# Optimization experiments

Hardware: AMD Instinct MI355X
Metric: run time of the kernel (lower is better)

The kernel has to match this reference:

```python
import jax, jax.numpy as jnp
import numpy as np

B, CIN, H, W = 32, 1, 512, 512
PATCH = 16
PW, PH = H // PATCH, W // PATCH  # 32, 32
S = PW * PH                      # 1024 tokens
C = 256
L = 8
POOL = 4
OUT_IDX = (2, 4, 6)
EPS = 1e-5


def setup_inputs() -> dict:
    key = jax.random.key(0)
    ks = jax.random.split(key, 10)
    sc = 1.0 / np.sqrt(C).astype(np.float32)
    return {
        "image": jax.random.normal(ks[0], (B, CIN, H, W), jnp.float32),
        "conv_w": jax.random.normal(ks[1], (C, CIN), jnp.float32),
        "conv_b": jnp.zeros((C,), jnp.float32),
        "feat_w": jax.random.normal(ks[2], (C, C), jnp.float32) * sc,
        "feat_b": jnp.zeros((C,), jnp.float32),
        "ln_s": jnp.ones((L, C), jnp.float32),
        "ln_b": jnp.zeros((L, C), jnp.float32),
        "wq": jax.random.normal(ks[3], (L, C, C), jnp.float32) * sc,
        "bq": jnp.zeros((L, C), jnp.float32),
        "wk": jax.random.normal(ks[4], (L, C, C), jnp.float32) * sc,
        "bk": jnp.zeros((L, C), jnp.float32),
        "wv": jax.random.normal(ks[5], (L, C, C), jnp.float32) * sc,
        "bv": jnp.zeros((L, C), jnp.float32),
        "wf": jax.random.normal(ks[6], (L, C, C), jnp.float32) * sc,
        "bf": jnp.zeros((L, C), jnp.float32),
        "wa": jax.random.normal(ks[7], (L, C, 2 * C), jnp.float32) * sc,
        "ba": jnp.zeros((L, 2 * C), jnp.float32),
    }


def _to_spatial(t):  # [B,S,C] -> [B,C,PW,PH]
    return t.transpose(0, 2, 1).reshape(t.shape[0], C, PW, PH)


def _to_seq(t):  # [B,C,PW,PH] -> [B,S,C]
    return t.reshape(t.shape[0], C, S).transpose(0, 2, 1)


def _layernorm(x, s, b):
    mu = x.mean(-1, keepdims=True)
    var = x.var(-1, keepdims=True)
    return (x - mu) * jax.lax.rsqrt(var + EPS) * s + b


def _attention(x, Wq, bq, Wk, bk, Wv, bv):
    d = np.float32(1.0 / np.sqrt(C))
    Q = _to_spatial(jax.nn.sigmoid(x @ Wq + bq))
    K = _to_spatial(jax.nn.sigmoid(x @ Wk + bk))
    V = _to_spatial(jax.nn.sigmoid(x @ Wv + bv))
    # avg_pool2d with kernel (POOL, 1): pool rows of the patch grid
    qp = Q.reshape(B, C, PW // POOL, POOL, PH).mean(3)
    kp = K.reshape(B, C, PW // POOL, POOL, PH).mean(3)
    # dual softmax low-rank factorization, per channel
    Qk = jax.nn.softmax(d * jnp.einsum('ncik,ncjk->ncij', Q, kp), axis=-1)   # [B,C,PW,PW/POOL]
    Kq = jax.nn.softmax(d * jnp.einsum('ncik,ncjk->ncij', qp, K), axis=-1)   # [B,C,PW/POOL,PW]
    Kqv = jnp.einsum('ncik,nckj->ncij', Kq, V)                               # [B,C,PW/POOL,PH]
    return _to_seq(jnp.einsum('ncik,nckj->ncij', Qk, Kqv))                   # [B,S,C]


def _forward(image, conv_w, conv_b, feat_w, feat_b, ln_s, ln_b,
             wq, bq, wk, bk, wv, bv, wf, bf, wa, ba):
    # Conv2d(kernel=1, stride=patch) == strided subsample + 1x1 projection
    xs = image[:, :, ::PATCH, ::PATCH]                                       # [B,1,PW,PH]
    emb = jnp.einsum('bihw,oi->bohw', xs, conv_w) + conv_b[None, :, None, None]
    x = jnp.tanh(_to_seq(emb) @ feat_w + feat_b)                             # [B,S,C]
    hid, att = [], []
    for l in range(L):
        tn = _layernorm(x, ln_s[l], ln_b[l])
        a = _attention(tn, wq[l], bq[l], wk[l], bk[l], wv[l], bv[l])
        ta = x + a
        # FiLM adaptive norm: sigmoid linear -> interleaved (scale, shift) pairs
        sh = jax.nn.sigmoid(ta @ wa[l] + ba[l]).reshape(B, S, C, 2)
        tn2 = sh[..., 0] * ta + sh[..., 1]
        x = jax.nn.relu(tn2 @ wf[l] + bf[l]) + ta
        if l in OUT_IDX:
            hid.append(x)
            att.append(ta)
    # pack: [last; 3 intermediate hiddens; 3 attention residuals] -> [7,B,S,C]
    return jnp.concatenate([x[None], jnp.stack(hid), jnp.stack(att)], axis=0)


def reference(image, conv_w, conv_b, feat_w, feat_b, ln_s, ln_b,
              wq, bq, wk, bk, wv, bv, wf, bf, wa, ba):
    return _forward(image, conv_w, conv_b, feat_w, feat_b, ln_s, ln_b,
                    wq, bq, wk, bk, wv, bv, wf, bf, wa, ba)
```

## Files before the change

### kernel.cpp

```cpp
#include <hip/hip_runtime.h>
#include <hip/hip_bf16.h>
#include <cstdint>
#include <cstddef>

#define B_ 32
#define C_ 256
#define S_ 1024
#define L_ 8

typedef unsigned short bf16_t;
typedef __attribute__((ext_vector_type(8))) short s8v;
typedef __attribute__((ext_vector_type(4))) short s4v;
typedef __attribute__((ext_vector_type(4))) float f4v;

static __device__ __forceinline__ float b2f(bf16_t v) {
    unsigned int u = ((unsigned int)v) << 16;
    float f;
    __builtin_memcpy(&f, &u, 4);
    return f;
}
static __device__ __forceinline__ bf16_t f2b(float f) {
    unsigned int u;
    __builtin_memcpy(&u, &f, 4);
    u += 0x7fffu + ((u >> 16) & 1u);
    return (bf16_t)(u >> 16);
}
static __device__ __forceinline__ float sigmoidf_(float x) {
    return 1.0f / (1.0f + __expf(-x));
}
static __device__ __forceinline__ void gload_lds16(const void* g, void* l) {
    __builtin_amdgcn_global_load_lds((const __attribute__((address_space(1))) void*)g,
                                     (__attribute__((address_space(3))) void*)l, 16, 0, 0);
}


__global__ void make_xs_k(const float* __restrict__ img, float* __restrict__ xs) {
    int t = blockIdx.x * 256 + threadIdx.x;
    if (t >= B_ * S_) return;
    int b = t >> 10, s = t & 1023, i = s >> 5, k = s & 31;
    xs[t] = img[(size_t)b * 512 * 512 + (size_t)(i * 16) * 512 + k * 16];
}

__global__ void fuse_wb_k(const float* __restrict__ cw, const float* __restrict__ cb,
                          const float* __restrict__ fwm, const float* __restrict__ fbv,
                          float* __restrict__ fw, float* __restrict__ fb) {
    int c = threadIdx.x;
    float a = 0.f, bs = 0.f;
    for (int o = 0; o < C_; o++) {
        float f = fwm[o * C_ + c];
        a += cw[o] * f;
        bs += cb[o] * f;
    }
    fw[c] = a;
    fb[c] = bs + fbv[c];
}

__global__ __launch_bounds__(256) void wtrans_k(const float* __restrict__ wq, const float* __restrict__ wk,
                                                const float* __restrict__ wv, const float* __restrict__ wf,
                                                const float* __restrict__ wa, const float* __restrict__ ln_s,
                                                bf16_t* __restrict__ WT) {
    __shared__ float t[32][33];
    int z = blockIdx.z, l = z / 6, tp = z - l * 6;
    const float* src;
    int ld, cmul, coff;
    if (tp < 4) {
        const float* bases[4] = {wq, wk, wv, wf};
        src = bases[tp] + (size_t)l * 65536;
        ld = 256; cmul = 1; coff = 0;
    } else {
        src = wa + (size_t)l * 131072;
        ld = 512; cmul = 2; coff = tp - 4;
    }
    const float* g = ln_s + l * 256;
    bf16_t* dst = WT + ((size_t)l * 6 + tp) * 65536;
    int k0 = blockIdx.y * 32, m0 = blockIdx.x * 32;
    int tx = threadIdx.x & 31, ty = threadIdx.x >> 5;
#pragma unroll
    for (int r = 0; r < 4; ++r) {
        int k = k0 + ty + 8 * r;
        float v = src[(size_t)k * ld + (m0 + tx) * cmul + coff];
        if (tp < 3) v *= g[k];
        t[ty + 8 * r][tx] = v;
    }
    __syncthreads();
#pragma unroll
    for (int r = 0; r < 4; ++r)
        dst[(size_t)(m0 + ty + 8 * r) * 256 + k0 + tx] = f2b(t[tx][ty + 8 * r]);
}

__global__ __launch_bounds__(256) void colsum_k(const bf16_t* __restrict__ WT,
                                                const float* __restrict__ wq, const float* __restrict__ wk,
                                                const float* __restrict__ wv,
                                                const float* __restrict__ bq, const float* __restrict__ bk,
                                                const float* __restrict__ bv,
                                                const float* __restrict__ ln_b,
                                                float* __restrict__ csum, float* __restrict__ bias2) {
    int m = threadIdx.x, mat = blockIdx.x, l = blockIdx.y;
    const bf16_t* wt = WT + ((size_t)l * 6 + mat) * 65536 + (size_t)m * 256;
    float cs = 0.f;
    for (int k = 0; k < 256; k += 8) {
        s8v u = *(const s8v*)(wt + k);
#pragma unroll
        for (int j = 0; j < 8; ++j) cs += b2f((bf16_t)u[j]);
    }
    const float* worig = (mat == 0 ? wq : mat == 1 ? wk : wv) + (size_t)l * 65536;
    const float* borig = (mat == 0 ? bq : mat == 1 ? bk : bv) + l * 256;
    const float* lb = ln_b + l * 256;
    float bb = 0.f;
    for (int k = 0; k < 256; ++k) bb += lb[k] * worig[(size_t)k * 256 + m];
    int o = (l * 3 + mat) * 256 + m;
    csum[o] = cs;
    bias2[o] = bb + borig[m];
}

__global__ __launch_bounds__(256) void embed_k(const float* __restrict__ xs, const float* __restrict__ fw,
                                               const float* __restrict__ fb, bf16_t* __restrict__ X,
                                               float* __restrict__ rs, float* __restrict__ rsmu) {
    int wid = threadIdx.x >> 6, lane = threadIdx.x & 63;
    int row = blockIdx.x * 4 + wid;
    float xv = xs[row];
    f4v fwv = *(const f4v*)(fw + lane * 4);
    f4v fbv = *(const f4v*)(fb + lane * 4);
    s4v o;
    float sum = 0.f, sq = 0.f;
#pragma unroll
    for (int j = 0; j < 4; ++j) {
        float v = tanhf(xv * fwv[j] + fbv[j]);
        float vb = b2f(f2b(v));
        o[j] = (short)f2b(v);
        sum += vb;
        sq += vb * vb;
    }
    *(s4v*)(X + (size_t)row * 256 + lane * 4) = o;
#pragma unroll
    for (int off = 32; off > 0; off >>= 1) {
        sum += __shfl_xor(sum, off);
        sq += __shfl_xor(sq, off);
    }
    if (lane == 0) {
        float mu = sum * (1.f / 256.f);
        float var = sq * (1.f / 256.f) - mu * mu;
        float r = rsqrtf(var + 1e-5f);
        rs[row] = r;
        rsmu[row] = r * mu;
    }
}

__global__ __launch_bounds__(256) void stats_k(const bf16_t* __restrict__ X,
                                               float* __restrict__ rs, float* __restrict__ rsmu) {
    int wid = threadIdx.x >> 6, lane = threadIdx.x & 63;
    int row2 = blockIdx.x * 8 + wid * 2;
    s8v v = *(const s8v*)(X + (size_t)row2 * 256 + lane * 8);
    float sum = 0.f, sq = 0.f;
#pragma unroll
    for (int j = 0; j < 8; ++j) {
        float f = b2f((bf16_t)v[j]);
        sum += f;
        sq += f * f;
    }
#pragma unroll
    for (int off = 16; off > 0; off >>= 1) {
        sum += __shfl_xor(sum, off);
        sq += __shfl_xor(sq, off);
    }
    if ((lane & 31) == 0) {
        int row = row2 + (lane >> 5);
        float mu = sum * (1.f / 256.f);
        float var = sq * (1.f / 256.f) - mu * mu;
        float r = rsqrtf(var + 1e-5f);
        rs[row] = r;
        rsmu[row] = r * mu;
    }
}

template <int MODE, bool HID>
__global__ __launch_bounds__(256) void mm_k(const bf16_t* Ain,
                                            const bf16_t* __restrict__ W0,
                                            const bf16_t* __restrict__ W1,
                                            const float* __restrict__ bias0,
                                            const float* __restrict__ csP,
                                            const float* __restrict__ rs,
                                            const float* __restrict__ rsmu,
                                            const bf16_t* ta,
                                            bf16_t* O0, bf16_t* O1, bf16_t* O2,
                                            float* __restrict__ hid) {
    constexpr int LDSZ = (MODE == 0) ? 34816 : 32768;
    __shared__ char lds[LDSZ];
    char* XS = lds;
    char* WS0 = lds + 16384;
    char* WS1 = lds + 24576;
    const int tid = threadIdx.x, lane = tid & 63, wid = tid >> 6;
    const int wrow = wid >> 1, wcol = wid & 1;
    const int s0 = blockIdx.y * 128, mt0 = blockIdx.x * 64, b = blockIdx.z;

    const int lr8 = lane >> 3;
    const int cb0 = ((lane & 7) << 4) ^ (lr8 << 4);

    const char* Ag = (const char*)Ain + (((size_t)b * 1024 + s0) * 256) * 2 + cb0;
    const char* Wg0 = (const char*)W0 + ((size_t)mt0 * 256) * 2 + cb0;
    const char* Wg1 = (const char*)W1 + ((size_t)mt0 * 256) * 2 + cb0;

    f4v acc[4][2] = {};
    f4v acc1[4][2] = {};

    for (int kt = 0; kt < 4; ++kt) {
        const char* ga = Ag + kt * 128;
#pragma unroll
        for (int q = 0; q < 4; ++q) {
            int r0 = wid * 32 + q * 8;
            gload_lds16(ga + (size_t)(r0 + lr8) * 512, XS + r0 * 128);
        }
        const char* gw = Wg0 + kt * 128;
#pragma unroll
        for (int p = 0; p < 2; ++p) {
            int r0 = wid * 16 + p * 8;
            gload_lds16(gw + (size_t)(r0 + lr8) * 512, WS0 + r0 * 128);
        }
        if constexpr (MODE == 1) {
            const char* gw1 = Wg1 + kt * 128;
#pragma unroll
            for (int p = 0; p < 2; ++p) {
                int r0 = wid * 16 + p * 8;
                gload_lds16(gw1 + (size_t)(r0 + lr8) * 512, WS1 + r0 * 128);
            }
        }
        __syncthreads();
#pragma unroll
        for (int kk = 0; kk < 2; ++kk) {
            const int cb = kk * 64 + ((lane >> 4) << 4);
            s8v av[4];
#pragma unroll
            for (int mi = 0; mi < 4; ++mi) {
                int r = wrow * 64 + mi * 16 + (lane & 15);
                av[mi] = *(const s8v*)(XS + r * 128 + (cb ^ ((r & 7) << 4)));
            }
            s8v bv[2], bw[2];
#pragma unroll
            for (int ni = 0; ni < 2; ++ni) {
                int m = wcol * 32 + ni * 16 + (lane & 15);
                bv[ni] = *(const s8v*)(WS0 + m * 128 + (cb ^ ((m & 7) << 4)));
                if constexpr (MODE == 1)
                    bw[ni] = *(const s8v*)(WS1 + m * 128 + (cb ^ ((m & 7) << 4)));
            }
#pragma unroll
            for (int mi = 0; mi < 4; ++mi)
#pragma unroll
                for (int ni = 0; ni < 2; ++ni) {
                    acc[mi][ni] = __builtin_amdgcn_mfma_f32_16x16x32_bf16(av[mi], bv[ni], acc[mi][ni], 0, 0, 0);
                    if constexpr (MODE == 1)
                        acc1[mi][ni] = __builtin_amdgcn_mfma_f32_16x16x32_bf16(av[mi], bw[ni], acc1[mi][ni], 0, 0, 0);
                }
        }
        __syncthreads();
    }

    if constexpr (MODE == 0) {
        const int mat = mt0 >> 8, mw = mt0 & 255;
        const float* bs = bias0 + mat * 256 + mw;
        const float* cs = csP + mat * 256 + mw;
        bf16_t* Os = (mat == 0) ? O0 : (mat == 1 ? O1 : O2);
        bf16_t* T = (bf16_t*)lds;
#pragma unroll
        for (int mi = 0; mi < 4; ++mi)
#pragma unroll
            for (int r = 0; r < 4; ++r) {
                int sl = wrow * 64 + mi * 16 + (lane >> 4) * 4 + r;
                int sg = b * 1024 + s0 + sl;
                float a = rs[sg], cc = rsmu[sg];
#pragma unroll
                for (int ni = 0; ni < 2; ++ni) {
                    int ml = wcol * 32 + ni * 16 + (lane & 15);
                    float v = sigmoidf_(a * acc[mi][ni][r] - cc * cs[ml] + bs[ml]);
                    T[ml * 144 + sl] = f2b(v);
                }
            }
        __syncthreads();
        int m = tid >> 2, c0s = (tid & 3) * 32;
        bf16_t* dst = Os + ((size_t)(b * 256 + mw + m)) * 1024 + s0 + c0s;
#pragma unroll
        for (int j = 0; j < 4; ++j)
            *(s8v*)(dst + j * 8) = *(const s8v*)(T + m * 144 + c0s + j * 8);
    } else {
#pragma unroll
        for (int mi = 0; mi < 4; ++mi)
#pragma unroll
            for (int ni = 0; ni < 2; ++ni) {
                int ml = mt0 + wcol * 32 + ni * 16 + (lane & 15);
#pragma unroll
                for (int r = 0; r < 4; ++r) {
                    int sg = b * 1024 + s0 + wrow * 64 + mi * 16 + (lane >> 4) * 4 + r;
                    size_t idx = (size_t)sg * 256 + ml;
                    if constexpr (MODE == 1) {
                        float v = sigmoidf_(acc[mi][ni][r] + bias0[2 * ml]) * b2f(ta[idx]) +
                                  sigmoidf_(acc1[mi][ni][r] + bias0[2 * ml + 1]);
                        O0[idx] = f2b(v);
                    } else {
                        float v = fmaxf(acc[mi][ni][r] + bias0[ml], 0.f) + b2f(ta[idx]);
                        O0[idx] = f2b(v);
                        if constexpr (HID) hid[idx] = v;
                    }
                }
            }
    }
}

__global__ __launch_bounds__(256) void attn_k(const bf16_t* __restrict__ Q, const bf16_t* __restrict__ K,
                                              const bf16_t* __restrict__ V, bf16_t* __restrict__ A) {
    __shared__ char Lds[35840];
    const int w = threadIdx.x >> 6, lane = threadIdx.x & 63;
    char* P = Lds + w * 8960;
    const int gw = blockIdx.x * 4 + w;
    const int b = gw >> 8, c = gw & 255;
    const size_t base = ((size_t)b * 256 + c) * 1024;
    constexpr int VT = 0, S1 = 2560, S2 = 5120, KQ = 6400;
    const f4v zf = {0.f, 0.f, 0.f, 0.f};
    const int frow = lane & 15, fhalf = lane >> 4;
    const int fbyte = fhalf * 16;
    const bf16_t* Qg = Q + base;
    const bf16_t* Kg = K + base;
    const bf16_t* Vg = V + base;

    s8v aq0 = *(const s8v*)(Qg + frow * 32 + fhalf * 8);
    s8v aq1 = *(const s8v*)(Qg + (16 + frow) * 32 + fhalf * 8);
    s8v bk0 = *(const s8v*)(Kg + frow * 32 + fhalf * 8);
    s8v bk1 = *(const s8v*)(Kg + (16 + frow) * 32 + fhalf * 8);
    float accq[8], acck[8];
#pragma unroll
    for (int j = 0; j < 8; ++j) { accq[j] = 0.f; acck[j] = 0.f; }
#pragma unroll
    for (int pp = 0; pp < 4; ++pp) {
        int rr = 4 * frow + pp;
        if (rr > 31) rr = 31;
        s8v uq = *(const s8v*)(Qg + rr * 32 + fhalf * 8);
        s8v uk = *(const s8v*)(Kg + rr * 32 + fhalf * 8);
#pragma unroll
        for (int j = 0; j < 8; ++j) {
            accq[j] += b2f((bf16_t)uq[j]);
            acck[j] += b2f((bf16_t)uk[j]);
        }
    }
    s8v aqp, bkp;
#pragma unroll
    for (int j = 0; j < 8; ++j) {
        aqp[j] = (short)f2b(accq[j] * 0.25f);
        bkp[j] = (short)f2b(acck[j] * 0.25f);
    }
    {
        s8v v0 = *(const s8v*)(Vg + lane * 16);
        s8v v1 = *(const s8v*)(Vg + lane * 16 + 8);
        int pw = lane >> 1, ph0 = (lane & 1) * 16;
#pragma unroll
        for (int j = 0; j < 8; ++j) {
            *(bf16_t*)(P + VT + (ph0 + j) * 80 + pw * 2) = (bf16_t)(unsigned short)v0[j];
            *(bf16_t*)(P + VT + (ph0 + 8 + j) * 80 + pw * 2) = (bf16_t)(unsigned short)v1[j];
        }
    }
    if (lane < 32) {
#pragma unroll
        for (int q = 0; q < 4; ++q) *(f4v*)(P + S1 + lane * 80 + q * 16) = zf;
#pragma unroll
        for (int q = 0; q < 3; ++q) *(f4v*)(P + KQ + lane * 80 + 16 + q * 16) = zf;
    } else if (lane < 40) {
#pragma unroll
        for (int q = 0; q < 4; ++q) *(f4v*)(P + S2 + (lane - 24) * 80 + q * 16) = zf;
    }

    f4v s1a = __builtin_amdgcn_mfma_f32_16x16x32_bf16(aq0, bkp, zf, 0, 0, 0);
    f4v s1b = __builtin_amdgcn_mfma_f32_16x16x32_bf16(aq1, bkp, zf, 0, 0, 0);
    f4v s2a = __builtin_amdgcn_mfma_f32_16x16x32_bf16(aqp, bk0, zf, 0, 0, 0);
    f4v s2b = __builtin_amdgcn_mfma_f32_16x16x32_bf16(aqp, bk1, zf, 0, 0, 0);

    const float dsc = 0.0625f;
    {
        int j = lane & 15;
#pragma unroll
        for (int t = 0; t < 2; ++t) {
            f4v av = t ? s1b : s1a;
#pragma unroll
            for (int r = 0; r < 4; ++r) {
                float x = av[r] * dsc;
                float m = x;
                m = fmaxf(m, __shfl_xor(m, 1));
                m = fmaxf(m, __shfl_xor(m, 2));
                m = fmaxf(m, __shfl_xor(m, 4));
                float e2 = __expf(x - m);
                float s = e2;
                s += __shfl_xor(s, 1);
                s += __shfl_xor(s, 2);
                s += __shfl_xor(s, 4);
                float p = e2 / s;
                if (j < 8) {
                    int row = t * 16 + fhalf * 4 + r;
                    *(bf16_t*)(P + S1 + row * 80 + j * 2) = f2b(p);
                }
            }
        }
    }
#pragma unroll
    for (int r = 0; r < 4; ++r) {
        float xa = s2a[r] * dsc, xb = s2b[r] * dsc;
        float m = fmaxf(xa, xb);
        m = fmaxf(m, __shfl_xor(m, 1));
        m = fmaxf(m, __shfl_xor(m, 2));
        m = fmaxf(m, __shfl_xor(m, 4));
        m = fmaxf(m, __shfl_xor(m, 8));
        float ea = __expf(xa - m), eb = __expf(xb - m);
        float s = ea + eb;
        s += __shfl_xor(s, 1);
        s += __shfl_xor(s, 2);
        s += __shfl_xor(s, 4);
        s += __shfl_xor(s, 8);
        float inv = 1.f / s;
        if (lane < 32) {
            int row = fhalf * 4 + r;
            *(bf16_t*)(P + S2 + row * 80 + frow * 2) = f2b(ea * inv);
            *(bf16_t*)(P + S2 + row * 80 + (16 + frow) * 2) = f2b(eb * inv);
        }
    }
    __builtin_amdgcn_wave_barrier();
    {
        s8v as2 = *(const s8v*)(P + S2 + frow * 80 + fbyte);
        s8v bv0 = *(const s8v*)(P + VT + frow * 80 + fbyte);
        s8v bv1 = *(const s8v*)(P + VT + (16 + frow) * 80 + fbyte);
        f4v k3a = __builtin_amdgcn_mfma_f32_16x16x32_bf16(as2, bv0, zf, 0, 0, 0);
        f4v k3b = __builtin_amdgcn_mfma_f32_16x16x32_bf16(as2, bv1, zf, 0, 0, 0);
        if (lane < 32) {
#pragma unroll
            for (int r = 0; r < 4; ++r) {
                int i2 = fhalf * 4 + r;
                *(bf16_t*)(P + KQ + frow * 80 + i2 * 2) = f2b(k3a[r]);
                *(bf16_t*)(P + KQ + (16 + frow) * 80 + i2 * 2) = f2b(k3b[r]);
            }
        }
    }
    __builtin_amdgcn_wave_barrier();
    {
        s8v a40 = *(const s8v*)(P + S1 + frow * 80 + fbyte);
        s8v a41 = *(const s8v*)(P + S1 + (16 + frow) * 80 + fbyte);
        s8v b40 = *(const s8v*)(P + KQ + frow * 80 + fbyte);
        s8v b41 = *(const s8v*)(P + KQ + (16 + frow) * 80 + fbyte);
        f4v o00 = __builtin_amdgcn_mfma_f32_16x16x32_bf16(a40, b40, zf, 0, 0, 0);
        f4v o01 = __builtin_amdgcn_mfma_f32_16x16x32_bf16(a40, b41, zf, 0, 0, 0);
        f4v o10 = __builtin_amdgcn_mfma_f32_16x16x32_bf16(a41, b40, zf, 0, 0, 0);
        f4v o11 = __builtin_amdgcn_mfma_f32_16x16x32_bf16(a41, b41, zf, 0, 0, 0);
#pragma unroll
        for (int r = 0; r < 4; ++r) {
            int r0 = fhalf * 4 + r;
            *(bf16_t*)(P + VT + r0 * 80 + frow * 2) = f2b(o00[r]);
            *(bf16_t*)(P + VT + r0 * 80 + (16 + frow) * 2) = f2b(o01[r]);
            *(bf16_t*)(P + VT + (16 + r0) * 80 + frow * 2) = f2b(o10[r]);
            *(bf16_t*)(P + VT + (16 + r0) * 80 + (16 + frow) * 2) = f2b(o11[r]);
        }
    }
    __builtin_amdgcn_wave_barrier();
    {
        int i = lane >> 1, hh = (lane & 1) * 32;
        s8v r0 = *(const s8v*)(P + VT + i * 80 + hh);
        s8v r1 = *(const s8v*)(P + VT + i * 80 + hh + 16);
        *(s8v*)(A + base + lane * 16) = r0;
        *(s8v*)(A + base + lane * 16 + 8) = r1;
    }
}

template <bool SNAP>
__global__ __launch_bounds__(256) void add_tr_k(const bf16_t* __restrict__ Aa, bf16_t* X,
                                                float* __restrict__ att) {
    __shared__ float T[32][33];
    int b = blockIdx.z, c0 = blockIdx.y * 32, s0 = blockIdx.x * 32;
    int tx = threadIdx.x & 31, ty = threadIdx.x >> 5;
#pragma unroll
    for (int r = 0; r < 4; ++r)
        T[ty + 8 * r][tx] = b2f(Aa[((size_t)(b * 256 + c0 + ty + 8 * r)) * 1024 + s0 + tx]);
    __syncthreads();
#pragma unroll
    for (int r = 0; r < 4; ++r) {
        int s = s0 + ty + 8 * r;
        size_t idx = ((size_t)(b * 1024 + s)) * 256 + c0 + tx;
        float v = b2f(X[idx]) + T[tx][ty + 8 * r];
        X[idx] = f2b(v);
        if constexpr (SNAP) att[idx] = v;
    }
}


extern "C" void kernel_launch(void* const* d_in, const int* in_sizes, int n_in,
                              void* d_out, int out_size, void* d_ws, size_t ws_size,
                              hipStream_t stream) {
    const float* image  = (const float*)d_in[0];
    const float* conv_w = (const float*)d_in[1];
    const float* conv_b = (const float*)d_in[2];
    const float* feat_w = (const float*)d_in[3];
    const float* feat_b = (const float*)d_in[4];
    const float* ln_s   = (const float*)d_in[5];
    const float* ln_b   = (const float*)d_in[6];
    const float* wq     = (const float*)d_in[7];
    const float* bq     = (const float*)d_in[8];
    const float* wk     = (const float*)d_in[9];
    const float* bk     = (const float*)d_in[10];
    const float* wv     = (const float*)d_in[11];
    const float* bv     = (const float*)d_in[12];
    const float* wf     = (const float*)d_in[13];
    const float* bfv    = (const float*)d_in[14];
    const float* wa     = (const float*)d_in[15];
    const float* ba     = (const float*)d_in[16];
    float* out = (float*)d_out;

    char* p = (char*)d_ws;
    const size_t MB16 = (size_t)B_ * S_ * C_ * sizeof(bf16_t);
    float* xs    = (float*)p;  p += 131072;
    float* fw    = (float*)p;  p += 1024;
    float* fb    = (float*)p;  p += 1024;
    float* rsb   = (float*)p;  p += 131072;
    float* rsmub = (float*)p;  p += 131072;
    float* csum  = (float*)p;  p += 24576;
    float* bias2 = (float*)p;  p += 24576;
    bf16_t* WT = (bf16_t*)p;   p += (size_t)48 * 65536 * 2;
    bf16_t* X  = (bf16_t*)p;   p += MB16;
    bf16_t* T1 = (bf16_t*)p;   p += MB16;
    bf16_t* T2 = (bf16_t*)p;   p += MB16;
    bf16_t* Qb = (bf16_t*)p;   p += MB16;
    bf16_t* Kb = (bf16_t*)p;   p += MB16;
    bf16_t* Vb = (bf16_t*)p;   p += MB16;
    size_t needed = (size_t)(p - (char*)d_ws);
    if (ws_size < needed) Vb = (bf16_t*)d_out;

    make_xs_k<<<128, 256, 0, stream>>>(image, xs);
    fuse_wb_k<<<1, 256, 0, stream>>>(conv_w, conv_b, feat_w, feat_b, fw, fb);
    wtrans_k<<<dim3(8, 8, 48), 256, 0, stream>>>(wq, wk, wv, wf, wa, ln_s, WT);
    colsum_k<<<dim3(3, 8), 256, 0, stream>>>(WT, wq, wk, wv, bq, bk, bv, ln_b, csum, bias2);
    embed_k<<<8192, 256, 0, stream>>>(xs, fw, fb, X, rsb, rsmub);

    const size_t slot = (size_t)B_ * S_ * C_;

    for (int l = 0; l < L_; ++l) {
        const bf16_t* WTl = WT + (size_t)l * 6 * 65536;
        int snap = (l == 2) ? 0 : (l == 4) ? 1 : (l == 6) ? 2 : -1;

        if (l > 0) stats_k<<<4096, 256, 0, stream>>>(X, rsb, rsmub);
        mm_k<0, false><<<dim3(12, 8, 32), 256, 0, stream>>>(
            X, WTl, nullptr, bias2 + l * 768, csum + l * 768, rsb, rsmub, nullptr, Qb, Kb, Vb, nullptr);
        attn_k<<<2048, 256, 0, stream>>>(Qb, Kb, Vb, T1);
        if (snap >= 0)
            add_tr_k<true><<<dim3(32, 8, 32), 256, 0, stream>>>(T1, X, out + (size_t)(4 + snap) * slot);
        else
            add_tr_k<false><<<dim3(32, 8, 32), 256, 0, stream>>>(T1, X, nullptr);
        mm_k<1, false><<<dim3(4, 8, 32), 256, 0, stream>>>(
            X, WTl + 4 * 65536, WTl + 5 * 65536, ba + l * 512, nullptr, nullptr, nullptr, X, T2, nullptr, nullptr, nullptr);
        float* hid = (snap >= 0) ? out + (size_t)(1 + snap) * slot : (l == 7 ? out : nullptr);
        if (hid)
            mm_k<2, true><<<dim3(4, 8, 32), 256, 0, stream>>>(
                T2, WTl + 3 * 65536, nullptr, bfv + l * 256, nullptr, nullptr, nullptr, X, X, nullptr, nullptr, hid);
        else
            mm_k<2, false><<<dim3(4, 8, 32), 256, 0, stream>>>(
                T2, WTl + 3 * 65536, nullptr, bfv + l * 256, nullptr, nullptr, nullptr, X, X, nullptr, nullptr, nullptr);
    }
}
```

Measured before the change: 1.140 ms.

## Fuse layernorm row statistics into FFN epilogue via atomics, drop stats kernel

Per-row sum and sum-of-squares for the next layer's layernorm are now accumulated in the FFN matmul epilogue with shuffle reductions and float atomics, into a double-buffered stats array. The mean and rsqrt are computed inside the QKV matmul prologue. This removes the separate stats pass that re-read the hidden state each layer. The strided image gather is also folded into the embed kernel. The cost is atomic traffic, and the statistics come from fp32 values rather than the rounded bf16 values, which changes rounding slightly.

```diff
diff --git a/kernel.cpp b/kernel.cpp
--- a/kernel.cpp
+++ b/kernel.cpp
@@ -33,13 +33,6 @@
                                      (__attribute__((address_space(3))) void*)l, 16, 0, 0);
 }
 
-
-__global__ void make_xs_k(const float* __restrict__ img, float* __restrict__ xs) {
-    int t = blockIdx.x * 256 + threadIdx.x;
-    if (t >= B_ * S_) return;
-    int b = t >> 10, s = t & 1023, i = s >> 5, k = s & 31;
-    xs[t] = img[(size_t)b * 512 * 512 + (size_t)(i * 16) * 512 + k * 16];
-}
 
 __global__ void fuse_wb_k(const float* __restrict__ cw, const float* __restrict__ cb,
                           const float* __restrict__ fwm, const float* __restrict__ fbv,
@@ -113,12 +106,13 @@
     bias2[o] = bb + borig[m];
 }
 
-__global__ __launch_bounds__(256) void embed_k(const float* __restrict__ xs, const float* __restrict__ fw,
+__global__ __launch_bounds__(256) void embed_k(const float* __restrict__ img, const float* __restrict__ fw,
                                                const float* __restrict__ fb, bf16_t* __restrict__ X,
-                                               float* __restrict__ rs, float* __restrict__ rsmu) {
+                                               float* __restrict__ SUM0, float* __restrict__ SUM1) {
     int wid = threadIdx.x >> 6, lane = threadIdx.x & 63;
     int row = blockIdx.x * 4 + wid;
-    float xv = xs[row];
+    int b = row >> 10, s = row & 1023;
+    float xv = img[(size_t)b * 262144 + (size_t)(s >> 5) * 8192 + (s & 31) * 16];
     f4v fwv = *(const f4v*)(fw + lane * 4);
     f4v fbv = *(const f4v*)(fb + lane * 4);
     s4v o;
@@ -138,38 +132,10 @@
         sq += __shfl_xor(sq, off);
     }
     if (lane == 0) {
-        float mu = sum * (1.f / 256.f);
-        float var = sq * (1.f / 256.f) - mu * mu;
-        float r = rsqrtf(var + 1e-5f);
-        rs[row] = r;
-        rsmu[row] = r * mu;
-    }
-}
-
-__global__ __launch_bounds__(256) void stats_k(const bf16_t* __restrict__ X,
-                                               float* __restrict__ rs, float* __restrict__ rsmu) {
-    int wid = threadIdx.x >> 6, lane = threadIdx.x & 63;
-    int row2 = blockIdx.x * 8 + wid * 2;
-    s8v v = *(const s8v*)(X + (size_t)row2 * 256 + lane * 8);
-    float sum = 0.f, sq = 0.f;
-#pragma unroll
-    for (int j = 0; j < 8; ++j) {
-        float f = b2f((bf16_t)v[j]);
-        sum += f;
-        sq += f * f;
-    }
-#pragma unroll
-    for (int off = 16; off > 0; off >>= 1) {
-        sum += __shfl_xor(sum, off);
-        sq += __shfl_xor(sq, off);
-    }
-    if ((lane & 31) == 0) {
-        int row = row2 + (lane >> 5);
-        float mu = sum * (1.f / 256.f);
-        float var = sq * (1.f / 256.f) - mu * mu;
-        float r = rsqrtf(var + 1e-5f);
-        rs[row] = r;
-        rsmu[row] = r * mu;
+        SUM0[2 * row] = sum;
+        SUM0[2 * row + 1] = sq;
+        SUM1[2 * row] = 0.f;
+        SUM1[2 * row + 1] = 0.f;
     }
 }
 
@@ -179,11 +145,12 @@
                                             const bf16_t* __restrict__ W1,
                                             const float* __restrict__ bias0,
                                             const float* __restrict__ csP,
-                                            const float* __restrict__ rs,
-                                            const float* __restrict__ rsmu,
+                                            const float* __restrict__ sumIn,
                                             const bf16_t* ta,
                                             bf16_t* O0, bf16_t* O1, bf16_t* O2,
-                                            float* __restrict__ hid) {
+                                            float* __restrict__ hid,
+                                            float* __restrict__ sumOut,
+                                            float* __restrict__ sumZero) {
     constexpr int LDSZ = (MODE == 0) ? 34816 : 32768;
     __shared__ char lds[LDSZ];
     char* XS = lds;
@@ -193,6 +160,11 @@
     const int wrow = wid >> 1, wcol = wid & 1;
     const int s0 = blockIdx.y * 128, mt0 = blockIdx.x * 64, b = blockIdx.z;
 
+    if constexpr (MODE == 2) {
+        int bid = ((blockIdx.z * gridDim.y) + blockIdx.y) * gridDim.x + blockIdx.x;
+        if (tid < 64) sumZero[bid * 64 + tid] = 0.f;
+    }
+
     const int lr8 = lane >> 3;
     const int cb0 = ((lane & 7) << 4) ^ (lr8 << 4);
 
@@ -266,7 +238,11 @@
             for (int r = 0; r < 4; ++r) {
                 int sl = wrow * 64 + mi * 16 + (lane >> 4) * 4 + r;
                 int sg = b * 1024 + s0 + sl;
-                float a = rs[sg], cc = rsmu[sg];
+                float2 sv = *(const float2*)(sumIn + 2 * sg);
+                float mu = sv.x * (1.f / 256.f);
+                float var = sv.y * (1.f / 256.f) - mu * mu;
+                float rsv = rsqrtf(var + 1e-5f);
+                float a = rsv, cc = rsv * mu;
 #pragma unroll
                 for (int ni = 0; ni < 2; ++ni) {
                     int ml = wcol * 32 + ni * 16 + (lane & 15);
@@ -280,7 +256,7 @@
 #pragma unroll
         for (int j = 0; j < 4; ++j)
             *(s8v*)(dst + j * 8) = *(const s8v*)(T + m * 144 + c0s + j * 8);
-    } else {
+    } else if constexpr (MODE == 1) {
 #pragma unroll
         for (int mi = 0; mi < 4; ++mi)
 #pragma unroll
@@ -290,15 +266,36 @@
                 for (int r = 0; r < 4; ++r) {
                     int sg = b * 1024 + s0 + wrow * 64 + mi * 16 + (lane >> 4) * 4 + r;
                     size_t idx = (size_t)sg * 256 + ml;
-                    if constexpr (MODE == 1) {
-                        float v = sigmoidf_(acc[mi][ni][r] + bias0[2 * ml]) * b2f(ta[idx]) +
-                                  sigmoidf_(acc1[mi][ni][r] + bias0[2 * ml + 1]);
-                        O0[idx] = f2b(v);
-                    } else {
-                        float v = fmaxf(acc[mi][ni][r] + bias0[ml], 0.f) + b2f(ta[idx]);
-                        O0[idx] = f2b(v);
-                        if constexpr (HID) hid[idx] = v;
-                    }
+                    float v = sigmoidf_(acc[mi][ni][r] + bias0[2 * ml]) * b2f(ta[idx]) +
+                              sigmoidf_(acc1[mi][ni][r] + bias0[2 * ml + 1]);
+                    O0[idx] = f2b(v);
+                }
+            }
+    } else {
+#pragma unroll
+        for (int mi = 0; mi < 4; ++mi)
+#pragma unroll
+            for (int r = 0; r < 4; ++r) {
+                int sg = b * 1024 + s0 + wrow * 64 + mi * 16 + (lane >> 4) * 4 + r;
+                float vv[2];
+#pragma unroll
+                for (int ni = 0; ni < 2; ++ni) {
+                    int ml = mt0 + wcol * 32 + ni * 16 + (lane & 15);
+                    size_t idx = (size_t)sg * 256 + ml;
+                    float v = fmaxf(acc[mi][ni][r] + bias0[ml], 0.f) + b2f(ta[idx]);
+                    O0[idx] = f2b(v);
+                    if constexpr (HID) hid[idx] = v;
+                    vv[ni] = v;
+                }
+                float ps = vv[0] + vv[1];
+                float pq = vv[0] * vv[0] + vv[1] * vv[1];
+                ps += __shfl_xor(ps, 1); pq += __shfl_xor(pq, 1);
+                ps += __shfl_xor(ps, 2); pq += __shfl_xor(pq, 2);
+                ps += __shfl_xor(ps, 4); pq += __shfl_xor(pq, 4);
+                ps += __shfl_xor(ps, 8); pq += __shfl_xor(pq, 8);
+                if ((lane & 15) == 0) {
+                    atomicAdd(&sumOut[2 * sg], ps);
+                    atomicAdd(&sumOut[2 * sg + 1], pq);
                 }
             }
     }
@@ -507,11 +504,9 @@
 
     char* p = (char*)d_ws;
     const size_t MB16 = (size_t)B_ * S_ * C_ * sizeof(bf16_t);
-    float* xs    = (float*)p;  p += 131072;
     float* fw    = (float*)p;  p += 1024;
     float* fb    = (float*)p;  p += 1024;
-    float* rsb   = (float*)p;  p += 131072;
-    float* rsmub = (float*)p;  p += 131072;
+    float* SUM   = (float*)p;  p += 524288;
     float* csum  = (float*)p;  p += 24576;
     float* bias2 = (float*)p;  p += 24576;
     bf16_t* WT = (bf16_t*)p;   p += (size_t)48 * 65536 * 2;
@@ -524,34 +519,39 @@
     size_t needed = (size_t)(p - (char*)d_ws);
     if (ws_size < needed) Vb = (bf16_t*)d_out;
 
-    make_xs_k<<<128, 256, 0, stream>>>(image, xs);
     fuse_wb_k<<<1, 256, 0, stream>>>(conv_w, conv_b, feat_w, feat_b, fw, fb);
     wtrans_k<<<dim3(8, 8, 48), 256, 0, stream>>>(wq, wk, wv, wf, wa, ln_s, WT);
     colsum_k<<<dim3(3, 8), 256, 0, stream>>>(WT, wq, wk, wv, bq, bk, bv, ln_b, csum, bias2);
-    embed_k<<<8192, 256, 0, stream>>>(xs, fw, fb, X, rsb, rsmub);
+    embed_k<<<8192, 256, 0, stream>>>(image, fw, fb, X, SUM, SUM + 65536);
 
     const size_t slot = (size_t)B_ * S_ * C_;
 
     for (int l = 0; l < L_; ++l) {
         const bf16_t* WTl = WT + (size_t)l * 6 * 65536;
         int snap = (l == 2) ? 0 : (l == 4) ? 1 : (l == 6) ? 2 : -1;
-
-        if (l > 0) stats_k<<<4096, 256, 0, stream>>>(X, rsb, rsmub);
+        const float* sumIn = SUM + (size_t)(l & 1) * 65536;
+        float* sumOut = SUM + (size_t)((l + 1) & 1) * 65536;
+        float* sumZero = SUM + (size_t)(l & 1) * 65536;
+
         mm_k<0, false><<<dim3(12, 8, 32), 256, 0, stream>>>(
-            X, WTl, nullptr, bias2 + l * 768, csum + l * 768, rsb, rsmub, nullptr, Qb, Kb, Vb, nullptr);
+            X, WTl, nullptr, bias2 + l * 768, csum + l * 768, sumIn, nullptr,
+            Qb, Kb, Vb, nullptr, nullptr, nullptr);
         attn_k<<<2048, 256, 0, stream>>>(Qb, Kb, Vb, T1);
         if (snap >= 0)
             add_tr_k<true><<<dim3(32, 8, 32), 256, 0, stream>>>(T1, X, out + (size_t)(4 + snap) * slot);
         else
             add_tr_k<false><<<dim3(32, 8, 32), 256, 0, stream>>>(T1, X, nullptr);
         mm_k<1, false><<<dim3(4, 8, 32), 256, 0, stream>>>(
-            X, WTl + 4 * 65536, WTl + 5 * 65536, ba + l * 512, nullptr, nullptr, nullptr, X, T2, nullptr, nullptr, nullptr);
+            X, WTl + 4 * 65536, WTl + 5 * 65536, ba + l * 512, nullptr, nullptr, X,
+            T2, nullptr, nullptr, nullptr, nullptr, nullptr);
         float* hid = (snap >= 0) ? out + (size_t)(1 + snap) * slot : (l == 7 ? out : nullptr);
         if (hid)
             mm_k<2, true><<<dim3(4, 8, 32), 256, 0, stream>>>(
-                T2, WTl + 3 * 65536, nullptr, bfv + l * 256, nullptr, nullptr, nullptr, X, X, nullptr, nullptr, hid);
+                T2, WTl + 3 * 65536, nullptr, bfv + l * 256, nullptr, nullptr, X,
+                X, nullptr, nullptr, hid, sumOut, sumZero);
         else
             mm_k<2, false><<<dim3(4, 8, 32), 256, 0, stream>>>(
-                T2, WTl + 3 * 65536, nullptr, bfv + l * 256, nullptr, nullptr, nullptr, X, X, nullptr, nullptr, nullptr);
-    }
-}
+                T2, WTl + 3 * 65536, nullptr, bfv + l * 256, nullptr, nullptr, X,
+                X, nullptr, nullptr, nullptr, sumOut, sumZero);
+    }
+}
```

Measured after the change: 1.148 ms. About the same (+0.7%).
